# Kernel tuning notes

Measured on AMD Instinct MI355X. Metric: run time of the kernel, lower is better.

The kernel has to match this reference:

```python
import jax, jax.numpy as jnp
import numpy as np

B, S, D = 8, 2048, 1024
NEG_INF = jnp.float32(-1e30)  # stand-in for -inf; rows with all-masked are overwritten anyway


def setup_inputs() -> dict:
    key = jax.random.key(0)
    ks = jax.random.split(key, 10)
    query = jax.random.normal(ks[0], (B, S, D), dtype=jnp.float32)
    key_t = jax.random.normal(ks[1], (B, S, D), dtype=jnp.float32)
    value = jax.random.normal(ks[2], (B, S, D), dtype=jnp.float32)
    # pad mask: prefix of valid tokens per batch element (realistic ragged batch)
    lengths = jax.random.randint(ks[3], (B,), S // 2, S + 1)
    pad_masks = jnp.arange(S)[None, :] < lengths[:, None]  # (B, S) bool
    # causal mask, same lower-triangular pattern per batch element
    causal = jnp.tril(jnp.ones((S, S), dtype=bool))
    causal_masks = jnp.broadcast_to(causal, (B, S, S))
    # Linear params (torch nn.Linear: y = x @ W.T + b)
    scale = 0.02
    Wq = jax.random.normal(ks[4], (D, D), dtype=jnp.float32) * scale
    bq = jnp.zeros((D,), dtype=jnp.float32)
    Wk = jax.random.normal(ks[5], (D, D), dtype=jnp.float32) * scale
    bk = jnp.zeros((D,), dtype=jnp.float32)
    Wv = jax.random.normal(ks[6], (D, D), dtype=jnp.float32) * scale
    bv = jnp.zeros((D,), dtype=jnp.float32)
    return {"query": query, "key": key_t, "value": value,
            "pad_masks": pad_masks, "causal_masks": causal_masks,
            "Wq": Wq, "bq": bq, "Wk": Wk, "bk": bk, "Wv": Wv, "bv": bv}


def reference(query, key, value, pad_masks, causal_masks, Wq, bq, Wk, bk, Wv, bv):
    d_model = query.shape[-1]
    Q = jnp.einsum('bsd,ed->bse', query, Wq) + bq
    K = jnp.einsum('bsd,ed->bse', key, Wk) + bk
    V = jnp.einsum('bsd,ed->bse', value, Wv) + bv
    scores = jnp.einsum('bqd,bkd->bqk', Q, K) / jnp.sqrt(jnp.float32(d_model))
    combined = pad_masks[:, None, :] & causal_masks              # (B, S, S)
    row_any = jnp.any(combined, axis=-1, keepdims=True)          # (B, S, 1)
    scores = jnp.where(combined, scores, NEG_INF)
    scores = jnp.where(row_any, scores, jnp.zeros_like(scores))
    attn = jax.nn.softmax(scores, axis=-1)
    attn = jnp.where(row_any, attn, jnp.zeros_like(attn))
    # multiply by pad mask along the QUERY axis (faithful to the torch transpose)
    attn = attn * pad_masks[:, :, None].astype(attn.dtype)
    seq_emds = jnp.einsum('bqk,bkd->bqd', attn, V)
    return seq_emds, attn
```

## Files before the change

kernel.cpp:

```cpp
#include <hip/hip_runtime.h>
#include <hip/hip_bf16.h>

#define B_ 8
#define S_ 2048
#define D_ 1024
#define SCALE 0.03125f

typedef __attribute__((ext_vector_type(4))) float f32x4;
typedef __attribute__((ext_vector_type(8))) short short8;
typedef __attribute__((ext_vector_type(4))) short short4v;

static __device__ inline unsigned short f2bf(float f) {
    unsigned int u = __float_as_uint(f);
    u += 0x7FFF + ((u >> 16) & 1);
    return (unsigned short)(u >> 16);
}

static __device__ __forceinline__ void gload16(const void* g, void* l) {
    __builtin_amdgcn_global_load_lds(
        (const __attribute__((address_space(1))) unsigned int*)g,
        (__attribute__((address_space(3))) unsigned int*)l, 16, 0, 0);
}

static __device__ __forceinline__ int xcd_swz(int hw, int nwg) {
    return (hw & 7) * (nwg >> 3) + (hw >> 3);
}

__global__ void lengths_kernel(const unsigned char* __restrict__ pm, int* __restrict__ lens) {
    __shared__ int cnt[B_];
    int tid = threadIdx.x;
    if (tid < B_) cnt[tid] = 0;
    __syncthreads();
    int layout;
    if (pm[0] == 1 && pm[1] == 1) layout = 0;
    else if (pm[0] == 1) layout = 1;
    else layout = 2;
    for (int i = tid; i < B_ * S_; i += blockDim.x) {
        bool v;
        if (layout == 0) v = pm[i] != 0;
        else if (layout == 1) v = ((const int*)pm)[i] != 0;
        else v = ((const float*)pm)[i] != 0.0f;
        if (v) atomicAdd(&cnt[i >> 11], 1);
    }
    __syncthreads();
    if (tid < B_) lens[tid] = cnt[tid];
}

__global__ void convert_all_kernel(const float* __restrict__ q, const float* __restrict__ k,
                                   const float* __restrict__ v,
                                   const float* __restrict__ Wq, const float* __restrict__ Wk,
                                   const float* __restrict__ Wv,
                                   unsigned short* __restrict__ Xb,
                                   unsigned short* __restrict__ Wb) {
    const int z = blockIdx.z;
    const float* src;
    unsigned short* dst;
    int n;
    if (z < 3) {
        src = (z == 0) ? q : (z == 1) ? k : v;
        dst = Xb + (size_t)z * B_ * S_ * D_;
        n = B_ * S_ * D_;
    } else {
        src = (z == 3) ? Wq : (z == 4) ? Wk : Wv;
        dst = Wb + (size_t)(z - 3) * D_ * D_;
        n = D_ * D_;
    }
    int idx = (blockIdx.x * 256 + threadIdx.x) * 8;
    if (idx >= n) return;
    float4 a = *(const float4*)(src + idx);
    float4 b = *(const float4*)(src + idx + 4);
    short8 o;
    o[0] = (short)f2bf(a.x); o[1] = (short)f2bf(a.y);
    o[2] = (short)f2bf(a.z); o[3] = (short)f2bf(a.w);
    o[4] = (short)f2bf(b.x); o[5] = (short)f2bf(b.y);
    o[6] = (short)f2bf(b.z); o[7] = (short)f2bf(b.w);
    *(short8*)(dst + idx) = o;
}

__global__ void proj_bf16_kernel(const unsigned short* __restrict__ Xb3,
                                 const unsigned short* __restrict__ Wb3,
                                 const float* __restrict__ bq, const float* __restrict__ bk,
                                 const float* __restrict__ bv,
                                 unsigned short* __restrict__ Qb,
                                 unsigned short* __restrict__ Kb,
                                 unsigned short* __restrict__ Vt) {
    const int log_id = xcd_swz(blockIdx.x, 3 * (B_ * S_ / 128) * (D_ / 128));
    const int z = log_id >> 10;
    const int rem = log_id & 1023;
    const int m0 = (rem >> 3) * 128;
    const int n0 = (rem & 7) * 128;

    const unsigned short* Xb = Xb3 + (size_t)z * B_ * S_ * D_;
    const unsigned short* Wb = Wb3 + (size_t)z * D_ * D_;
    const float* bias = (z == 0) ? bq : (z == 1) ? bk : bv;

    __shared__ unsigned short As[128 * 32];
    __shared__ unsigned short Bs[128 * 32];

    const int tid = threadIdx.x;
    const int lane = tid & 63, w = tid >> 6;
    const int wr = w >> 1, wc = w & 1;
    const int g = lane >> 4, l15 = lane & 15;

    f32x4 acc[4][4];
    const f32x4 z4 = {0.f, 0.f, 0.f, 0.f};
    for (int a = 0; a < 4; ++a)
        for (int b2 = 0; b2 < 4; ++b2) acc[a][b2] = z4;

    for (int kk = 0; kk < D_; kk += 32) {
#pragma unroll
        for (int t = 0; t < 2; ++t) {
            int flat = (w * 2 + t) * 1024 + lane * 16;
            int row = flat >> 6, colb = flat & 63;
            const char* ga = (const char*)Xb + ((size_t)(m0 + row) * D_ + kk) * 2 + colb;
            const char* gb = (const char*)Wb + ((size_t)(n0 + row) * D_ + kk) * 2 + colb;
            gload16(ga, (char*)As + (w * 2 + t) * 1024);
            gload16(gb, (char*)Bs + (w * 2 + t) * 1024);
        }
        asm volatile("s_waitcnt vmcnt(0)" ::: "memory");
        __syncthreads();
        short8 a_frag[4], b_frag[4];
#pragma unroll
        for (int mf = 0; mf < 4; ++mf)
            a_frag[mf] = *(const short8*)(&As[(wr * 64 + mf * 16 + l15) * 32 + g * 8]);
#pragma unroll
        for (int nf = 0; nf < 4; ++nf)
            b_frag[nf] = *(const short8*)(&Bs[(wc * 64 + nf * 16 + l15) * 32 + g * 8]);
#pragma unroll
        for (int mf = 0; mf < 4; ++mf)
#pragma unroll
            for (int nf = 0; nf < 4; ++nf)
                acc[mf][nf] = __builtin_amdgcn_mfma_f32_16x16x32_bf16(a_frag[mf], b_frag[nf], acc[mf][nf], 0, 0, 0);
        __syncthreads();
    }

    if (z < 2) {
        unsigned short* O = (z == 0) ? Qb : Kb;
#pragma unroll
        for (int mf = 0; mf < 4; ++mf) {
#pragma unroll
            for (int nf = 0; nf < 4; ++nf) {
                int gm = m0 + wr * 64 + mf * 16 + 4 * g;
                int gn = n0 + wc * 64 + nf * 16 + l15;
                float bb = bias[gn];
#pragma unroll
                for (int i = 0; i < 4; ++i)
                    O[(size_t)(gm + i) * D_ + gn] = f2bf(acc[mf][nf][i] + bb);
            }
        }
    } else {
#pragma unroll
        for (int mf = 0; mf < 4; ++mf) {
#pragma unroll
            for (int nf = 0; nf < 4; ++nf) {
                int gm = m0 + wr * 64 + mf * 16 + 4 * g;
                int b = gm >> 11, tok = gm & 2047;
                int gn = n0 + wc * 64 + nf * 16 + l15;
                float bb = bias[gn];
                short4v sv;
#pragma unroll
                for (int i = 0; i < 4; ++i) sv[i] = (short)f2bf(acc[mf][nf][i] + bb);
                *(short4v*)(&Vt[((size_t)b * D_ + gn) * S_ + tok]) = sv;
            }
        }
    }
}

__global__ void proj_kernel(const float* __restrict__ q, const float* __restrict__ k,
                            const float* __restrict__ v,
                            const float* __restrict__ Wq, const float* __restrict__ Wk,
                            const float* __restrict__ Wv,
                            const float* __restrict__ bq, const float* __restrict__ bk,
                            const float* __restrict__ bv,
                            unsigned short* __restrict__ Qb, unsigned short* __restrict__ Kb,
                            unsigned short* __restrict__ Vt) {
    const int z = blockIdx.z;
    const float* X = (z == 0) ? q : (z == 1) ? k : v;
    const float* W = (z == 0) ? Wq : (z == 1) ? Wk : Wv;
    const float* bias = (z == 0) ? bq : (z == 1) ? bk : bv;

    __shared__ short As[128 * 40];
    __shared__ short Bs[128 * 40];

    const int m0 = blockIdx.y * 128;
    const int n0 = blockIdx.x * 128;
    const int tid = threadIdx.x;
    const int lane = tid & 63, wid = tid >> 6;
    const int wr = wid >> 1, wc = wid & 1;
    const int g = lane >> 4, l15 = lane & 15;

    f32x4 acc[4][4];
    const f32x4 z4 = {0.f, 0.f, 0.f, 0.f};
    for (int a = 0; a < 4; ++a)
        for (int b2 = 0; b2 < 4; ++b2) acc[a][b2] = z4;

    for (int kk = 0; kk < D_; kk += 32) {
#pragma unroll
        for (int it = 0; it < 4; ++it) {
            int flat = it * 1024 + tid * 4;
            int r = flat >> 5, c = flat & 31;
            float4 va = *(const float4*)(X + (size_t)(m0 + r) * D_ + kk + c);
            short4v sa = {(short)f2bf(va.x), (short)f2bf(va.y), (short)f2bf(va.z), (short)f2bf(va.w)};
            *(short4v*)(&As[r * 40 + c]) = sa;
            float4 vb = *(const float4*)(W + (size_t)(n0 + r) * D_ + kk + c);
            short4v sb = {(short)f2bf(vb.x), (short)f2bf(vb.y), (short)f2bf(vb.z), (short)f2bf(vb.w)};
            *(short4v*)(&Bs[r * 40 + c]) = sb;
        }
        __syncthreads();
        short8 a_frag[4], b_frag[4];
#pragma unroll
        for (int mf = 0; mf < 4; ++mf)
            a_frag[mf] = *(const short8*)(&As[(wr * 64 + mf * 16 + l15) * 40 + g * 8]);
#pragma unroll
        for (int nf = 0; nf < 4; ++nf)
            b_frag[nf] = *(const short8*)(&Bs[(wc * 64 + nf * 16 + l15) * 40 + g * 8]);
#pragma unroll
        for (int mf = 0; mf < 4; ++mf)
#pragma unroll
            for (int nf = 0; nf < 4; ++nf)
                acc[mf][nf] = __builtin_amdgcn_mfma_f32_16x16x32_bf16(a_frag[mf], b_frag[nf], acc[mf][nf], 0, 0, 0);
        __syncthreads();
    }

    if (z < 2) {
        unsigned short* O = (z == 0) ? Qb : Kb;
#pragma unroll
        for (int mf = 0; mf < 4; ++mf) {
#pragma unroll
            for (int nf = 0; nf < 4; ++nf) {
                int gm = m0 + wr * 64 + mf * 16 + 4 * g;
                int gn = n0 + wc * 64 + nf * 16 + l15;
                float bb = bias[gn];
#pragma unroll
                for (int i = 0; i < 4; ++i)
                    O[(size_t)(gm + i) * D_ + gn] = f2bf(acc[mf][nf][i] + bb);
            }
        }
    } else {
#pragma unroll
        for (int mf = 0; mf < 4; ++mf) {
#pragma unroll
            for (int nf = 0; nf < 4; ++nf) {
                int gm = m0 + wr * 64 + mf * 16 + 4 * g;
                int b = gm >> 11, tok = gm & 2047;
                int gn = n0 + wc * 64 + nf * 16 + l15;
                float bb = bias[gn];
                short4v sv;
#pragma unroll
                for (int i = 0; i < 4; ++i) sv[i] = (short)f2bf(acc[mf][nf][i] + bb);
                *(short4v*)(&Vt[((size_t)b * D_ + gn) * S_ + tok]) = sv;
            }
        }
    }
}

__global__ void scores_kernel(const unsigned short* __restrict__ Qb,
                              const unsigned short* __restrict__ Kb,
                              const int* __restrict__ lens,
                              float* __restrict__ attn) {
    const int log_id = xcd_swz(blockIdx.x, 136 * B_);
    const int b = log_id / 136;
    const int idx = log_id - b * 136;
    int qt = (int)((sqrtf(8.f * idx + 1.f) - 1.f) * 0.5f);
    while ((qt + 1) * (qt + 2) / 2 <= idx) ++qt;
    while (qt * (qt + 1) / 2 > idx) --qt;
    const int kt = idx - qt * (qt + 1) / 2;
    const int m0 = qt * 128, n0 = kt * 128;
    const int len = lens[b];
    if (m0 >= len) return;

    __shared__ unsigned short As[128 * 32];
    __shared__ unsigned short Bs[128 * 32];

    const int tid = threadIdx.x;
    const int lane = tid & 63, w = tid >> 6;
    const int wr = w >> 1, wc = w & 1;
    const int g = lane >> 4, l15 = lane & 15;

    const char* Qbase = (const char*)(Qb + (size_t)(b * S_ + m0) * D_);
    const char* Kbase = (const char*)(Kb + (size_t)(b * S_ + n0) * D_);

    f32x4 acc[4][4];
    const f32x4 z4 = {0.f, 0.f, 0.f, 0.f};
    for (int a = 0; a < 4; ++a)
        for (int b2 = 0; b2 < 4; ++b2) acc[a][b2] = z4;

    for (int kk = 0; kk < D_; kk += 32) {
#pragma unroll
        for (int t = 0; t < 2; ++t) {
            int flat = (w * 2 + t) * 1024 + lane * 16;
            int row = flat >> 6, colb = flat & 63;
            gload16(Qbase + (size_t)row * (D_ * 2) + kk * 2 + colb, (char*)As + (w * 2 + t) * 1024);
            gload16(Kbase + (size_t)row * (D_ * 2) + kk * 2 + colb, (char*)Bs + (w * 2 + t) * 1024);
        }
        asm volatile("s_waitcnt vmcnt(0)" ::: "memory");
        __syncthreads();
        short8 a_frag[4], b_frag[4];
#pragma unroll
        for (int mf = 0; mf < 4; ++mf)
            a_frag[mf] = *(const short8*)(&As[(wr * 64 + mf * 16 + l15) * 32 + g * 8]);
#pragma unroll
        for (int nf = 0; nf < 4; ++nf)
            b_frag[nf] = *(const short8*)(&Bs[(wc * 64 + nf * 16 + l15) * 32 + g * 8]);
#pragma unroll
        for (int mf = 0; mf < 4; ++mf)
#pragma unroll
            for (int nf = 0; nf < 4; ++nf)
                acc[mf][nf] = __builtin_amdgcn_mfma_f32_16x16x32_bf16(a_frag[mf], b_frag[nf], acc[mf][nf], 0, 0, 0);
        __syncthreads();
    }

#pragma unroll
    for (int mf = 0; mf < 4; ++mf) {
#pragma unroll
        for (int nf = 0; nf < 4; ++nf) {
            int gm = m0 + wr * 64 + mf * 16 + 4 * g;
            int gn = n0 + wc * 64 + nf * 16 + l15;
#pragma unroll
            for (int i = 0; i < 4; ++i) {
                int rq = gm + i;
                if (rq < len && gn <= rq)
                    attn[(size_t)(b * S_ + rq) * S_ + gn] = acc[mf][nf][i] * SCALE;
            }
        }
    }
}

__global__ void softmax_kernel(const int* __restrict__ lens,
                               float* __restrict__ attn, unsigned short* __restrict__ P) {
    const int row = blockIdx.x;
    const int b = row >> 11, qpos = row & 2047;
    const int tid = threadIdx.x;
    const size_t rbase = (size_t)row * S_;
    const int c0 = tid * 8;
    if (qpos >= lens[b]) {
        short8 z = {0, 0, 0, 0, 0, 0, 0, 0};
        *(short8*)(&P[rbase + c0]) = z;
        const float4 zf = {0.f, 0.f, 0.f, 0.f};
        *(float4*)(attn + rbase + c0) = zf;
        *(float4*)(attn + rbase + c0 + 4) = zf;
        return;
    }
    __shared__ float wm[4], wl[4];
    float4 a0 = *(const float4*)(attn + rbase + c0);
    float4 a1 = *(const float4*)(attn + rbase + c0 + 4);
    float x[8] = {a0.x, a0.y, a0.z, a0.w, a1.x, a1.y, a1.z, a1.w};
    float lmax = -1e30f;
#pragma unroll
    for (int j = 0; j < 8; ++j) {
        if (c0 + j > qpos) x[j] = -1e30f;
        lmax = fmaxf(lmax, x[j]);
    }
#pragma unroll
    for (int off = 1; off < 64; off <<= 1) lmax = fmaxf(lmax, __shfl_xor(lmax, off));
    if ((tid & 63) == 0) wm[tid >> 6] = lmax;
    __syncthreads();
    const float m = fmaxf(fmaxf(wm[0], wm[1]), fmaxf(wm[2], wm[3]));
    float e[8];
    float lsum = 0.f;
#pragma unroll
    for (int j = 0; j < 8; ++j) {
        e[j] = (x[j] > -1e29f) ? __expf(x[j] - m) : 0.f;
        lsum += e[j];
    }
#pragma unroll
    for (int off = 1; off < 64; off <<= 1) lsum += __shfl_xor(lsum, off);
    if ((tid & 63) == 0) wl[tid >> 6] = lsum;
    __syncthreads();
    const float inv = 1.0f / (wl[0] + wl[1] + wl[2] + wl[3]);
    float4 o0, o1;
    short8 pb;
#pragma unroll
    for (int j = 0; j < 8; ++j) {
        e[j] *= inv;
        pb[j] = (short)f2bf(e[j]);
    }
    o0.x = e[0]; o0.y = e[1]; o0.z = e[2]; o0.w = e[3];
    o1.x = e[4]; o1.y = e[5]; o1.z = e[6]; o1.w = e[7];
    *(float4*)(attn + rbase + c0) = o0;
    *(float4*)(attn + rbase + c0 + 4) = o1;
    *(short8*)(&P[rbase + c0]) = pb;
}

__global__ void pv_kernel(const unsigned short* __restrict__ P,
                          const unsigned short* __restrict__ Vt,
                          const int* __restrict__ lens, float* __restrict__ seq) {
    const int log_id = xcd_swz(blockIdx.x, B_ * (S_ / 128) * (D_ / 128));
    const int b = log_id >> 7;
    const int rem = log_id & 127;
    const int q0 = (rem >> 3) * 128;
    const int n0 = (rem & 7) * 128;
    const int len = lens[b];
    const int tid = threadIdx.x;

    if (q0 >= len) {
        const float4 zf = {0.f, 0.f, 0.f, 0.f};
#pragma unroll
        for (int it = 0; it < 16; ++it) {
            int flat = it * 1024 + tid * 4;
            int r = flat >> 7, c = flat & 127;
            *(float4*)(&seq[(size_t)(b * S_ + q0 + r) * D_ + n0 + c]) = zf;
        }
        return;
    }

    __shared__ unsigned short As[128 * 32];
    __shared__ unsigned short Bs[128 * 32];
    const int lane = tid & 63, w = tid >> 6;
    const int wr = w >> 1, wc = w & 1;
    const int g = lane >> 4, l15 = lane & 15;

    f32x4 acc[4][4];
    const f32x4 z4 = {0.f, 0.f, 0.f, 0.f};
    for (int a = 0; a < 4; ++a)
        for (int b2 = 0; b2 < 4; ++b2) acc[a][b2] = z4;

    const char* Pbase = (const char*)(P + (size_t)(b * S_ + q0) * S_);
    const char* Vbase = (const char*)(Vt + ((size_t)b * D_ + n0) * S_);

    const int nkt = (q0 + 128) / 32;
    for (int kt = 0; kt < nkt; ++kt) {
        int k0 = kt * 32;
#pragma unroll
        for (int t = 0; t < 2; ++t) {
            int flat = (w * 2 + t) * 1024 + lane * 16;
            int row = flat >> 6, colb = flat & 63;
            gload16(Pbase + (size_t)row * (S_ * 2) + k0 * 2 + colb, (char*)As + (w * 2 + t) * 1024);
            gload16(Vbase + (size_t)row * (S_ * 2) + k0 * 2 + colb, (char*)Bs + (w * 2 + t) * 1024);
        }
        asm volatile("s_waitcnt vmcnt(0)" ::: "memory");
        __syncthreads();
        short8 a_frag[4], b_frag[4];
#pragma unroll
        for (int mf = 0; mf < 4; ++mf)
            a_frag[mf] = *(const short8*)(&As[(wr * 64 + mf * 16 + l15) * 32 + g * 8]);
#pragma unroll
        for (int nf = 0; nf < 4; ++nf)
            b_frag[nf] = *(const short8*)(&Bs[(wc * 64 + nf * 16 + l15) * 32 + g * 8]);
#pragma unroll
        for (int mf = 0; mf < 4; ++mf)
#pragma unroll
            for (int nf = 0; nf < 4; ++nf)
                acc[mf][nf] = __builtin_amdgcn_mfma_f32_16x16x32_bf16(a_frag[mf], b_frag[nf], acc[mf][nf], 0, 0, 0);
        __syncthreads();
    }

#pragma unroll
    for (int mf = 0; mf < 4; ++mf) {
#pragma unroll
        for (int nf = 0; nf < 4; ++nf) {
            int gq = q0 + wr * 64 + mf * 16 + 4 * g;
            int gn = n0 + wc * 64 + nf * 16 + l15;
#pragma unroll
            for (int i = 0; i < 4; ++i)
                seq[(size_t)(b * S_ + gq + i) * D_ + gn] = acc[mf][nf][i];
        }
    }
}

extern "C" void kernel_launch(void* const* d_in, const int* in_sizes, int n_in,
                              void* d_out, int out_size, void* d_ws, size_t ws_size,
                              hipStream_t stream) {
    const float* q = (const float*)d_in[0];
    const float* k = (const float*)d_in[1];
    const float* v = (const float*)d_in[2];
    const unsigned char* pm = (const unsigned char*)d_in[3];
    const float* Wq = (const float*)d_in[5];
    const float* bq = (const float*)d_in[6];
    const float* Wk = (const float*)d_in[7];
    const float* bk = (const float*)d_in[8];
    const float* Wv = (const float*)d_in[9];
    const float* bv = (const float*)d_in[10];

    float* seq = (float*)d_out;
    float* attn = seq + (size_t)B_ * S_ * D_;

    char* ws = (char*)d_ws;
    int* lens = (int*)ws;
    unsigned short* Qb = (unsigned short*)(ws + 256);
    unsigned short* Kb = Qb + (size_t)B_ * S_ * D_;
    unsigned short* Vt = Kb + (size_t)B_ * S_ * D_;
    unsigned short* Xb = Vt + (size_t)B_ * D_ * S_;
    unsigned short* Wb = Xb + 3ull * B_ * S_ * D_;
    unsigned short* P = Qb;

    const size_t need = 256 + 6ull * B_ * S_ * D_ * 2 + 3ull * D_ * D_ * 2;

    lengths_kernel<<<1, 256, 0, stream>>>(pm, lens);

    if (ws_size >= need) {
        convert_all_kernel<<<dim3(B_ * S_ * D_ / 2048, 1, 6), 256, 0, stream>>>(
            q, k, v, Wq, Wk, Wv, Xb, Wb);
        proj_bf16_kernel<<<dim3(3 * (B_ * S_ / 128) * (D_ / 128)), 256, 0, stream>>>(
            Xb, Wb, bq, bk, bv, Qb, Kb, Vt);
    } else {
        proj_kernel<<<dim3(D_ / 128, (B_ * S_) / 128, 3), 256, 0, stream>>>(
            q, k, v, Wq, Wk, Wv, bq, bk, bv, Qb, Kb, Vt);
    }

    scores_kernel<<<dim3(136 * B_), 256, 0, stream>>>(Qb, Kb, lens, attn);
    softmax_kernel<<<dim3(B_ * S_), 256, 0, stream>>>(lens, attn, P);
    pv_kernel<<<dim3(B_ * (S_ / 128) * (D_ / 128)), 256, 0, stream>>>(P, Vt, lens, seq);
}
```

Baseline: 412.2 us.

## Double-buffer LDS tiles in GEMM kernels and skip masked work in softmax

Result: no change. 405.2 us (-1.7%).

```diff
diff --git a/kernel.cpp b/kernel.cpp
--- a/kernel.cpp
+++ b/kernel.cpp
@@ -20,6 +20,12 @@
     __builtin_amdgcn_global_load_lds(
         (const __attribute__((address_space(1))) unsigned int*)g,
         (__attribute__((address_space(3))) unsigned int*)l, 16, 0, 0);
+}
+
+static __device__ __forceinline__ void pipe_sync() {
+    asm volatile("s_waitcnt vmcnt(0)" ::: "memory");
+    __builtin_amdgcn_s_barrier();
+    __builtin_amdgcn_sched_barrier(0);
 }
 
 static __device__ __forceinline__ int xcd_swz(int hw, int nwg) {
@@ -94,44 +100,52 @@
     const unsigned short* Wb = Wb3 + (size_t)z * D_ * D_;
     const float* bias = (z == 0) ? bq : (z == 1) ? bk : bv;
 
-    __shared__ unsigned short As[128 * 32];
-    __shared__ unsigned short Bs[128 * 32];
+    __shared__ unsigned short As[2][128 * 32];
+    __shared__ unsigned short Bs[2][128 * 32];
 
     const int tid = threadIdx.x;
     const int lane = tid & 63, w = tid >> 6;
     const int wr = w >> 1, wc = w & 1;
     const int g = lane >> 4, l15 = lane & 15;
 
+    const int flat0 = (w * 2 + 0) * 1024 + lane * 16;
+    const int flat1 = (w * 2 + 1) * 1024 + lane * 16;
+    const int r0 = flat0 >> 6, cb0 = flat0 & 63;
+    const int r1 = flat1 >> 6, cb1 = flat1 & 63;
+
+    auto stage = [&](int buf, int kk) {
+        gload16((const char*)Xb + ((size_t)(m0 + r0) * D_ + kk) * 2 + cb0, (char*)&As[buf][0] + flat0);
+        gload16((const char*)Xb + ((size_t)(m0 + r1) * D_ + kk) * 2 + cb1, (char*)&As[buf][0] + flat1);
+        gload16((const char*)Wb + ((size_t)(n0 + r0) * D_ + kk) * 2 + cb0, (char*)&Bs[buf][0] + flat0);
+        gload16((const char*)Wb + ((size_t)(n0 + r1) * D_ + kk) * 2 + cb1, (char*)&Bs[buf][0] + flat1);
+    };
+
     f32x4 acc[4][4];
     const f32x4 z4 = {0.f, 0.f, 0.f, 0.f};
     for (int a = 0; a < 4; ++a)
         for (int b2 = 0; b2 < 4; ++b2) acc[a][b2] = z4;
 
+    stage(0, 0);
+    pipe_sync();
+    int cur = 0;
     for (int kk = 0; kk < D_; kk += 32) {
-#pragma unroll
-        for (int t = 0; t < 2; ++t) {
-            int flat = (w * 2 + t) * 1024 + lane * 16;
-            int row = flat >> 6, colb = flat & 63;
-            const char* ga = (const char*)Xb + ((size_t)(m0 + row) * D_ + kk) * 2 + colb;
-            const char* gb = (const char*)Wb + ((size_t)(n0 + row) * D_ + kk) * 2 + colb;
-            gload16(ga, (char*)As + (w * 2 + t) * 1024);
-            gload16(gb, (char*)Bs + (w * 2 + t) * 1024);
-        }
-        asm volatile("s_waitcnt vmcnt(0)" ::: "memory");
-        __syncthreads();
+        if (kk + 32 < D_) stage(cur ^ 1, kk + 32);
         short8 a_frag[4], b_frag[4];
 #pragma unroll
         for (int mf = 0; mf < 4; ++mf)
-            a_frag[mf] = *(const short8*)(&As[(wr * 64 + mf * 16 + l15) * 32 + g * 8]);
+            a_frag[mf] = *(const short8*)(&As[cur][(wr * 64 + mf * 16 + l15) * 32 + g * 8]);
 #pragma unroll
         for (int nf = 0; nf < 4; ++nf)
-            b_frag[nf] = *(const short8*)(&Bs[(wc * 64 + nf * 16 + l15) * 32 + g * 8]);
+            b_frag[nf] = *(const short8*)(&Bs[cur][(wc * 64 + nf * 16 + l15) * 32 + g * 8]);
+        __builtin_amdgcn_s_setprio(1);
 #pragma unroll
         for (int mf = 0; mf < 4; ++mf)
 #pragma unroll
             for (int nf = 0; nf < 4; ++nf)
                 acc[mf][nf] = __builtin_amdgcn_mfma_f32_16x16x32_bf16(a_frag[mf], b_frag[nf], acc[mf][nf], 0, 0, 0);
-        __syncthreads();
+        __builtin_amdgcn_s_setprio(0);
+        pipe_sync();
+        cur ^= 1;
     }
 
     if (z < 2) {
@@ -269,8 +283,8 @@
     const int len = lens[b];
     if (m0 >= len) return;
 
-    __shared__ unsigned short As[128 * 32];
-    __shared__ unsigned short Bs[128 * 32];
+    __shared__ unsigned short As[2][128 * 32];
+    __shared__ unsigned short Bs[2][128 * 32];
 
     const int tid = threadIdx.x;
     const int lane = tid & 63, w = tid >> 6;
@@ -280,47 +294,72 @@
     const char* Qbase = (const char*)(Qb + (size_t)(b * S_ + m0) * D_);
     const char* Kbase = (const char*)(Kb + (size_t)(b * S_ + n0) * D_);
 
+    const int flat0 = (w * 2 + 0) * 1024 + lane * 16;
+    const int flat1 = (w * 2 + 1) * 1024 + lane * 16;
+    const int r0 = flat0 >> 6, cb0 = flat0 & 63;
+    const int r1 = flat1 >> 6, cb1 = flat1 & 63;
+
+    auto stage = [&](int buf, int kk) {
+        gload16(Qbase + (size_t)r0 * (D_ * 2) + kk * 2 + cb0, (char*)&As[buf][0] + flat0);
+        gload16(Qbase + (size_t)r1 * (D_ * 2) + kk * 2 + cb1, (char*)&As[buf][0] + flat1);
+        gload16(Kbase + (size_t)r0 * (D_ * 2) + kk * 2 + cb0, (char*)&Bs[buf][0] + flat0);
+        gload16(Kbase + (size_t)r1 * (D_ * 2) + kk * 2 + cb1, (char*)&Bs[buf][0] + flat1);
+    };
+
     f32x4 acc[4][4];
     const f32x4 z4 = {0.f, 0.f, 0.f, 0.f};
     for (int a = 0; a < 4; ++a)
         for (int b2 = 0; b2 < 4; ++b2) acc[a][b2] = z4;
 
+    stage(0, 0);
+    pipe_sync();
+    int cur = 0;
     for (int kk = 0; kk < D_; kk += 32) {
-#pragma unroll
-        for (int t = 0; t < 2; ++t) {
-            int flat = (w * 2 + t) * 1024 + lane * 16;
-            int row = flat >> 6, colb = flat & 63;
-            gload16(Qbase + (size_t)row * (D_ * 2) + kk * 2 + colb, (char*)As + (w * 2 + t) * 1024);
-            gload16(Kbase + (size_t)row * (D_ * 2) + kk * 2 + colb, (char*)Bs + (w * 2 + t) * 1024);
-        }
-        asm volatile("s_waitcnt vmcnt(0)" ::: "memory");
-        __syncthreads();
+        if (kk + 32 < D_) stage(cur ^ 1, kk + 32);
         short8 a_frag[4], b_frag[4];
 #pragma unroll
         for (int mf = 0; mf < 4; ++mf)
-            a_frag[mf] = *(const short8*)(&As[(wr * 64 + mf * 16 + l15) * 32 + g * 8]);
+            a_frag[mf] = *(const short8*)(&As[cur][(wr * 64 + mf * 16 + l15) * 32 + g * 8]);
 #pragma unroll
         for (int nf = 0; nf < 4; ++nf)
-            b_frag[nf] = *(const short8*)(&Bs[(wc * 64 + nf * 16 + l15) * 32 + g * 8]);
+            b_frag[nf] = *(const short8*)(&Bs[cur][(wc * 64 + nf * 16 + l15) * 32 + g * 8]);
+        __builtin_amdgcn_s_setprio(1);
 #pragma unroll
         for (int mf = 0; mf < 4; ++mf)
 #pragma unroll
             for (int nf = 0; nf < 4; ++nf)
                 acc[mf][nf] = __builtin_amdgcn_mfma_f32_16x16x32_bf16(a_frag[mf], b_frag[nf], acc[mf][nf], 0, 0, 0);
-        __syncthreads();
-    }
-
-#pragma unroll
-    for (int mf = 0; mf < 4; ++mf) {
-#pragma unroll
-        for (int nf = 0; nf < 4; ++nf) {
-            int gm = m0 + wr * 64 + mf * 16 + 4 * g;
-            int gn = n0 + wc * 64 + nf * 16 + l15;
-#pragma unroll
-            for (int i = 0; i < 4; ++i) {
-                int rq = gm + i;
-                if (rq < len && gn <= rq)
-                    attn[(size_t)(b * S_ + rq) * S_ + gn] = acc[mf][nf][i] * SCALE;
+        __builtin_amdgcn_s_setprio(0);
+        pipe_sync();
+        cur ^= 1;
+    }
+
+    const bool interior = (m0 >= n0 + 128) && (m0 + 128 <= len);
+    if (interior) {
+#pragma unroll
+        for (int mf = 0; mf < 4; ++mf) {
+#pragma unroll
+            for (int nf = 0; nf < 4; ++nf) {
+                int gm = m0 + wr * 64 + mf * 16 + 4 * g;
+                int gn = n0 + wc * 64 + nf * 16 + l15;
+#pragma unroll
+                for (int i = 0; i < 4; ++i)
+                    attn[(size_t)(b * S_ + gm + i) * S_ + gn] = acc[mf][nf][i] * SCALE;
+            }
+        }
+    } else {
+#pragma unroll
+        for (int mf = 0; mf < 4; ++mf) {
+#pragma unroll
+            for (int nf = 0; nf < 4; ++nf) {
+                int gm = m0 + wr * 64 + mf * 16 + 4 * g;
+                int gn = n0 + wc * 64 + nf * 16 + l15;
+#pragma unroll
+                for (int i = 0; i < 4; ++i) {
+                    int rq = gm + i;
+                    if (rq < len && gn <= rq)
+                        attn[(size_t)(b * S_ + rq) * S_ + gn] = acc[mf][nf][i] * SCALE;
+                }
             }
         }
     }
@@ -333,24 +372,32 @@
     const int tid = threadIdx.x;
     const size_t rbase = (size_t)row * S_;
     const int c0 = tid * 8;
+    const short8 zp = {0, 0, 0, 0, 0, 0, 0, 0};
+    const float4 zf = {0.f, 0.f, 0.f, 0.f};
     if (qpos >= lens[b]) {
-        short8 z = {0, 0, 0, 0, 0, 0, 0, 0};
-        *(short8*)(&P[rbase + c0]) = z;
-        const float4 zf = {0.f, 0.f, 0.f, 0.f};
+        *(short8*)(&P[rbase + c0]) = zp;
         *(float4*)(attn + rbase + c0) = zf;
         *(float4*)(attn + rbase + c0 + 4) = zf;
         return;
     }
     __shared__ float wm[4], wl[4];
-    float4 a0 = *(const float4*)(attn + rbase + c0);
-    float4 a1 = *(const float4*)(attn + rbase + c0 + 4);
-    float x[8] = {a0.x, a0.y, a0.z, a0.w, a1.x, a1.y, a1.z, a1.w};
+    const bool act = (c0 <= qpos);
+    float x[8];
+    if (act) {
+        float4 a0 = *(const float4*)(attn + rbase + c0);
+        float4 a1 = *(const float4*)(attn + rbase + c0 + 4);
+        x[0] = a0.x; x[1] = a0.y; x[2] = a0.z; x[3] = a0.w;
+        x[4] = a1.x; x[5] = a1.y; x[6] = a1.z; x[7] = a1.w;
+#pragma unroll
+        for (int j = 0; j < 8; ++j)
+            if (c0 + j > qpos) x[j] = -1e30f;
+    } else {
+#pragma unroll
+        for (int j = 0; j < 8; ++j) x[j] = -1e30f;
+    }
     float lmax = -1e30f;
 #pragma unroll
-    for (int j = 0; j < 8; ++j) {
-        if (c0 + j > qpos) x[j] = -1e30f;
-        lmax = fmaxf(lmax, x[j]);
-    }
+    for (int j = 0; j < 8; ++j) lmax = fmaxf(lmax, x[j]);
 #pragma unroll
     for (int off = 1; off < 64; off <<= 1) lmax = fmaxf(lmax, __shfl_xor(lmax, off));
     if ((tid & 63) == 0) wm[tid >> 6] = lmax;
@@ -367,19 +414,25 @@
     for (int off = 1; off < 64; off <<= 1) lsum += __shfl_xor(lsum, off);
     if ((tid & 63) == 0) wl[tid >> 6] = lsum;
     __syncthreads();
-    const float inv = 1.0f / (wl[0] + wl[1] + wl[2] + wl[3]);
-    float4 o0, o1;
-    short8 pb;
-#pragma unroll
-    for (int j = 0; j < 8; ++j) {
-        e[j] *= inv;
-        pb[j] = (short)f2bf(e[j]);
-    }
-    o0.x = e[0]; o0.y = e[1]; o0.z = e[2]; o0.w = e[3];
-    o1.x = e[4]; o1.y = e[5]; o1.z = e[6]; o1.w = e[7];
-    *(float4*)(attn + rbase + c0) = o0;
-    *(float4*)(attn + rbase + c0 + 4) = o1;
-    *(short8*)(&P[rbase + c0]) = pb;
+    if (act) {
+        const float inv = 1.0f / (wl[0] + wl[1] + wl[2] + wl[3]);
+        float4 o0, o1;
+        short8 pb;
+#pragma unroll
+        for (int j = 0; j < 8; ++j) {
+            e[j] *= inv;
+            pb[j] = (short)f2bf(e[j]);
+        }
+        o0.x = e[0]; o0.y = e[1]; o0.z = e[2]; o0.w = e[3];
+        o1.x = e[4]; o1.y = e[5]; o1.z = e[6]; o1.w = e[7];
+        *(float4*)(attn + rbase + c0) = o0;
+        *(float4*)(attn + rbase + c0 + 4) = o1;
+        *(short8*)(&P[rbase + c0]) = pb;
+    } else {
+        *(float4*)(attn + rbase + c0) = zf;
+        *(float4*)(attn + rbase + c0 + 4) = zf;
+        *(short8*)(&P[rbase + c0]) = zp;
+    }
 }
 
 __global__ void pv_kernel(const unsigned short* __restrict__ P,
@@ -404,45 +457,55 @@
         return;
     }
 
-    __shared__ unsigned short As[128 * 32];
-    __shared__ unsigned short Bs[128 * 32];
+    __shared__ unsigned short As[2][128 * 32];
+    __shared__ unsigned short Bs[2][128 * 32];
     const int lane = tid & 63, w = tid >> 6;
     const int wr = w >> 1, wc = w & 1;
     const int g = lane >> 4, l15 = lane & 15;
+
+    const char* Pbase = (const char*)(P + (size_t)(b * S_ + q0) * S_);
+    const char* Vbase = (const char*)(Vt + ((size_t)b * D_ + n0) * S_);
+
+    const int flat0 = (w * 2 + 0) * 1024 + lane * 16;
+    const int flat1 = (w * 2 + 1) * 1024 + lane * 16;
+    const int r0 = flat0 >> 6, cb0 = flat0 & 63;
+    const int r1 = flat1 >> 6, cb1 = flat1 & 63;
+
+    auto stage = [&](int buf, int k0) {
+        gload16(Pbase + (size_t)r0 * (S_ * 2) + k0 * 2 + cb0, (char*)&As[buf][0] + flat0);
+        gload16(Pbase + (size_t)r1 * (S_ * 2) + k0 * 2 + cb1, (char*)&As[buf][0] + flat1);
+        gload16(Vbase + (size_t)r0 * (S_ * 2) + k0 * 2 + cb0, (char*)&Bs[buf][0] + flat0);
+        gload16(Vbase + (size_t)r1 * (S_ * 2) + k0 * 2 + cb1, (char*)&Bs[buf][0] + flat1);
+    };
 
     f32x4 acc[4][4];
     const f32x4 z4 = {0.f, 0.f, 0.f, 0.f};
     for (int a = 0; a < 4; ++a)
         for (int b2 = 0; b2 < 4; ++b2) acc[a][b2] = z4;
 
-    const char* Pbase = (const char*)(P + (size_t)(b * S_ + q0) * S_);
-    const char* Vbase = (const char*)(Vt + ((size_t)b * D_ + n0) * S_);
-
     const int nkt = (q0 + 128) / 32;
+
+    stage(0, 0);
+    pipe_sync();
+    int cur = 0;
     for (int kt = 0; kt < nkt; ++kt) {
-        int k0 = kt * 32;
-#pragma unroll
-        for (int t = 0; t < 2; ++t) {
-            int flat = (w * 2 + t) * 1024 + lane * 16;
-            int row = flat >> 6, colb = flat & 63;
-            gload16(Pbase + (size_t)row * (S_ * 2) + k0 * 2 + colb, (char*)As + (w * 2 + t) * 1024);
-            gload16(Vbase + (size_t)row * (S_ * 2) + k0 * 2 + colb, (char*)Bs + (w * 2 + t) * 1024);
-        }
-        asm volatile("s_waitcnt vmcnt(0)" ::: "memory");
-        __syncthreads();
+        if (kt + 1 < nkt) stage(cur ^ 1, (kt + 1) * 32);
         short8 a_frag[4], b_frag[4];
 #pragma unroll
         for (int mf = 0; mf < 4; ++mf)
-            a_frag[mf] = *(const short8*)(&As[(wr * 64 + mf * 16 + l15) * 32 + g * 8]);
+            a_frag[mf] = *(const short8*)(&As[cur][(wr * 64 + mf * 16 + l15) * 32 + g * 8]);
 #pragma unroll
         for (int nf = 0; nf < 4; ++nf)
-            b_frag[nf] = *(const short8*)(&Bs[(wc * 64 + nf * 16 + l15) * 32 + g * 8]);
+            b_frag[nf] = *(const short8*)(&Bs[cur][(wc * 64 + nf * 16 + l15) * 32 + g * 8]);
+        __builtin_amdgcn_s_setprio(1);
 #pragma unroll
         for (int mf = 0; mf < 4; ++mf)
 #pragma unroll
             for (int nf = 0; nf < 4; ++nf)
                 acc[mf][nf] = __builtin_amdgcn_mfma_f32_16x16x32_bf16(a_frag[mf], b_frag[nf], acc[mf][nf], 0, 0, 0);
-        __syncthreads();
+        __builtin_amdgcn_s_setprio(0);
+        pipe_sync();
+        cur ^= 1;
     }
 
 #pragma unroll
```
